# Kernel tuning notes

Hardware: AMD Instinct MI355X
Metric: run time of the kernel (lower is better)

## Reference

```python
import jax, jax.numpy as jnp
import numpy as np

K, M, N = 8, 1024, 1024  # bits, in_features, out_features (nf)
B_, S_ = 4, 2048

def setup_inputs() -> dict:
    key = jax.random.key(0)
    k1, k2, k3, k4 = jax.random.split(key, 4)
    x = jax.random.normal(k1, (B_, S_, M), dtype=jnp.float32)
    # per-bit +/-1 sign matrices, stored as float (module casts int8 -> x.dtype)
    binary = jnp.where(jax.random.normal(k2, (K, M, N)) > 0, 1.0, -1.0).astype(jnp.float32)
    # positive per-bit, per-output-channel scales (sup decomposition yields positives)
    scale = jax.random.uniform(k3, (K, 1, N), dtype=jnp.float32, minval=0.01, maxval=1.0)
    bias = jax.random.normal(k4, (N,), dtype=jnp.float32)
    return {"x": x, "binary": binary, "scale": scale, "bias": bias}

def reference(x, binary, scale, bias):
    size_out = x.shape[:-1] + (N,)
    x2 = x.reshape(-1, x.shape[-1])                 # [T, m]
    # k separate dense matmuls against +/-1 matrices: [k, T, n]
    xk = jnp.einsum('tm,kmn->ktn', x2, binary)
    out = jnp.sum(xk * scale, axis=0)               # per-bit scale then sum over bits
    out = out + bias
    return out.reshape(size_out)
```

## Files before the change

### kernel.cpp

```cpp
#include <hip/hip_runtime.h>
#include <cstdint>

#define TDIM 8192
#define MDIM 1024
#define NDIM 1024
#define KBITS 8
#define BK 64
#define TT 64
#define TN 128

typedef __bf16 bf16x8 __attribute__((ext_vector_type(8)));
typedef float f32x4 __attribute__((ext_vector_type(4)));
typedef float f32x16 __attribute__((ext_vector_type(16)));

#define GAS(p) ((__attribute__((address_space(1))) void*)(uintptr_t)(p))
#define LAS(p) ((__attribute__((address_space(3))) void*)(uintptr_t)(p))

__device__ __forceinline__ unsigned short f2bf(float f) {
    union { float f; unsigned u; } v; v.f = f;
    unsigned r = v.u + 0x7fffu + ((v.u >> 16) & 1u);
    return (unsigned short)(r >> 16);
}

__global__ __launch_bounds__(256) void prep_kernel(const float* __restrict__ x,
                                                   unsigned short* __restrict__ xb,
                                                   const float* __restrict__ binary,
                                                   const float* __restrict__ scale,
                                                   unsigned short* __restrict__ wtr) {
    __shared__ float tile[32][33];
    const int tid = threadIdx.x;
    if (blockIdx.x >= 1024) {
        size_t idx = ((size_t)(blockIdx.x - 1024) * 256 + tid) * 8;
        float4 a = *(const float4*)(x + idx);
        float4 b = *(const float4*)(x + idx + 4);
        uint4 o;
        o.x = (unsigned)f2bf(a.x) | ((unsigned)f2bf(a.y) << 16);
        o.y = (unsigned)f2bf(a.z) | ((unsigned)f2bf(a.w) << 16);
        o.z = (unsigned)f2bf(b.x) | ((unsigned)f2bf(b.y) << 16);
        o.w = (unsigned)f2bf(b.z) | ((unsigned)f2bf(b.w) << 16);
        *(uint4*)(xb + idx) = o;
        return;
    }
    const int n0 = (blockIdx.x & 31) * 32;
    const int m0 = (blockIdx.x >> 5) * 32;
    const int r = tid >> 3;
    const int cn = (tid & 7) * 4;
    f32x4 acc = {0.f, 0.f, 0.f, 0.f};
#pragma unroll
    for (int k = 0; k < KBITS; ++k) {
        f32x4 v = *(const f32x4*)(binary + ((size_t)k * MDIM + m0 + r) * NDIM + n0 + cn);
        f32x4 s = *(const f32x4*)(scale + (size_t)k * NDIM + n0 + cn);
        acc += v * s;
    }
#pragma unroll
    for (int e = 0; e < 4; ++e) tile[cn + e][r] = acc[e];
    __syncthreads();
    const int rn = tid >> 3;
    const int cm = (tid & 7) * 4;
    ushort4 o4;
    o4.x = f2bf(tile[rn][cm + 0]);
    o4.y = f2bf(tile[rn][cm + 1]);
    o4.z = f2bf(tile[rn][cm + 2]);
    o4.w = f2bf(tile[rn][cm + 3]);
    *(ushort4*)(wtr + (size_t)(n0 + rn) * MDIM + m0 + cm) = o4;
}

__global__ __launch_bounds__(256, 4) void gemm_kernel(const unsigned short* __restrict__ xb,
                                                      const unsigned short* __restrict__ wtr,
                                                      const float* __restrict__ bias,
                                                      float* __restrict__ out) {
    __shared__ __attribute__((aligned(16))) unsigned short sA[TT * BK];
    __shared__ __attribute__((aligned(16))) unsigned short sB[TN * BK];

    const int tid = threadIdx.x;
    const int lane = tid & 63;
    const int wv = tid >> 6;
    const int wrow = wv >> 1;
    const int wcol = wv & 1;
    const int lr = lane & 31;
    const int half = lane >> 5;

    const int t0 = blockIdx.x * TT;
    const int n0 = blockIdx.y * TN;

    const unsigned short* srcA[2];
    unsigned short* dstA[2];
#pragma unroll
    for (int j = 0; j < 2; ++j) {
        int s = tid + j * 256;
        int r = s >> 3;
        int g = (s & 7) ^ (r & 7);
        srcA[j] = xb + (size_t)(t0 + r) * MDIM + g * 8;
        dstA[j] = sA + s * 8;
    }
    const unsigned short* srcB[4];
    unsigned short* dstB[4];
#pragma unroll
    for (int j = 0; j < 4; ++j) {
        int s = tid + j * 256;
        int r = s >> 3;
        int g = (s & 7) ^ (r & 7);
        srcB[j] = wtr + (size_t)(n0 + r) * MDIM + g * 8;
        dstB[j] = sB + s * 8;
    }

    int a_off[4], b_off[4][2];
#pragma unroll
    for (int c = 0; c < 4; ++c) {
        int m = wrow * 32 + lr;
        a_off[c] = (m * 8 + ((c * 2 + half) ^ (m & 7))) * 8;
#pragma unroll
        for (int j = 0; j < 2; ++j) {
            int n = wcol * 64 + j * 32 + lr;
            b_off[c][j] = (n * 8 + ((c * 2 + half) ^ (n & 7))) * 8;
        }
    }

    f32x16 acc[2];
#pragma unroll
    for (int j = 0; j < 2; ++j)
#pragma unroll
        for (int r = 0; r < 16; ++r) acc[j][r] = 0.f;

    for (int k0 = 0; k0 < MDIM; k0 += BK) {
#pragma unroll
        for (int j = 0; j < 2; ++j)
            __builtin_amdgcn_global_load_lds(GAS(srcA[j] + k0), LAS(dstA[j]), 16, 0, 0);
#pragma unroll
        for (int j = 0; j < 4; ++j)
            __builtin_amdgcn_global_load_lds(GAS(srcB[j] + k0), LAS(dstB[j]), 16, 0, 0);
        __syncthreads();

#pragma unroll
        for (int c = 0; c < 4; ++c) {
            bf16x8 af = *(const bf16x8*)(sA + a_off[c]);
            bf16x8 b0 = *(const bf16x8*)(sB + b_off[c][0]);
            bf16x8 b1 = *(const bf16x8*)(sB + b_off[c][1]);
            acc[0] = __builtin_amdgcn_mfma_f32_32x32x16_bf16(af, b0, acc[0], 0, 0, 0);
            acc[1] = __builtin_amdgcn_mfma_f32_32x32x16_bf16(af, b1, acc[1], 0, 0, 0);
        }
        __syncthreads();
    }

#pragma unroll
    for (int j = 0; j < 2; ++j) {
        const int n = n0 + wcol * 64 + j * 32 + lr;
        const float bv = bias[n];
#pragma unroll
        for (int r = 0; r < 16; ++r) {
            const int t = t0 + wrow * 32 + (r & 3) + 8 * (r >> 2) + 4 * half;
            out[(size_t)t * NDIM + n] = acc[j][r] + bv;
        }
    }
}

extern "C" void kernel_launch(void* const* d_in, const int* in_sizes, int n_in,
                              void* d_out, int out_size, void* d_ws, size_t ws_size,
                              hipStream_t stream) {
    const float* x      = (const float*)d_in[0];
    const float* binary = (const float*)d_in[1];
    const float* scale  = (const float*)d_in[2];
    const float* bias   = (const float*)d_in[3];
    float* out = (float*)d_out;

    unsigned short* xb  = (unsigned short*)d_ws;
    unsigned short* wtr = xb + (size_t)TDIM * MDIM;

    prep_kernel<<<1024 + 4096, 256, 0, stream>>>(x, xb, binary, scale, wtr);
    gemm_kernel<<<dim3(TDIM / TT, NDIM / TN), 256, 0, stream>>>(xb, wtr, bias, out);
}
```

Baseline: 128.0 us.

## Fuse x fp32-to-bf16 conversion into GEMM A-tile loading

```diff
diff --git a/kernel.cpp b/kernel.cpp
--- a/kernel.cpp
+++ b/kernel.cpp
@@ -22,25 +22,11 @@
     return (unsigned short)(r >> 16);
 }
 
-__global__ __launch_bounds__(256) void prep_kernel(const float* __restrict__ x,
-                                                   unsigned short* __restrict__ xb,
-                                                   const float* __restrict__ binary,
-                                                   const float* __restrict__ scale,
-                                                   unsigned short* __restrict__ wtr) {
+__global__ __launch_bounds__(256) void wfold_kernel(const float* __restrict__ binary,
+                                                    const float* __restrict__ scale,
+                                                    unsigned short* __restrict__ wtr) {
     __shared__ float tile[32][33];
     const int tid = threadIdx.x;
-    if (blockIdx.x >= 1024) {
-        size_t idx = ((size_t)(blockIdx.x - 1024) * 256 + tid) * 8;
-        float4 a = *(const float4*)(x + idx);
-        float4 b = *(const float4*)(x + idx + 4);
-        uint4 o;
-        o.x = (unsigned)f2bf(a.x) | ((unsigned)f2bf(a.y) << 16);
-        o.y = (unsigned)f2bf(a.z) | ((unsigned)f2bf(a.w) << 16);
-        o.z = (unsigned)f2bf(b.x) | ((unsigned)f2bf(b.y) << 16);
-        o.w = (unsigned)f2bf(b.z) | ((unsigned)f2bf(b.w) << 16);
-        *(uint4*)(xb + idx) = o;
-        return;
-    }
     const int n0 = (blockIdx.x & 31) * 32;
     const int m0 = (blockIdx.x >> 5) * 32;
     const int r = tid >> 3;
@@ -65,11 +51,11 @@
     *(ushort4*)(wtr + (size_t)(n0 + rn) * MDIM + m0 + cm) = o4;
 }
 
-__global__ __launch_bounds__(256, 4) void gemm_kernel(const unsigned short* __restrict__ xb,
+__global__ __launch_bounds__(256, 4) void gemm_kernel(const float* __restrict__ x,
                                                       const unsigned short* __restrict__ wtr,
                                                       const float* __restrict__ bias,
                                                       float* __restrict__ out) {
-    __shared__ __attribute__((aligned(16))) unsigned short sA[TT * BK];
+    __shared__ __attribute__((aligned(16))) float sAf[TT * BK];
     __shared__ __attribute__((aligned(16))) unsigned short sB[TN * BK];
 
     const int tid = threadIdx.x;
@@ -83,15 +69,15 @@
     const int t0 = blockIdx.x * TT;
     const int n0 = blockIdx.y * TN;
 
-    const unsigned short* srcA[2];
-    unsigned short* dstA[2];
+    const float* srcA[4];
+    float* dstA[4];
 #pragma unroll
-    for (int j = 0; j < 2; ++j) {
+    for (int j = 0; j < 4; ++j) {
         int s = tid + j * 256;
-        int r = s >> 3;
-        int g = (s & 7) ^ (r & 7);
-        srcA[j] = xb + (size_t)(t0 + r) * MDIM + g * 8;
-        dstA[j] = sA + s * 8;
+        int r = s >> 4;
+        int g = (s & 15) ^ (r & 15);
+        srcA[j] = x + (size_t)(t0 + r) * MDIM + g * 4;
+        dstA[j] = sAf + s * 4;
     }
     const unsigned short* srcB[4];
     unsigned short* dstB[4];
@@ -104,11 +90,12 @@
         dstB[j] = sB + s * 8;
     }
 
-    int a_off[4], b_off[4][2];
+    const int mrow = wrow * 32 + lr;
+    int a0_off[4], a1_off[4], b_off[4][2];
 #pragma unroll
     for (int c = 0; c < 4; ++c) {
-        int m = wrow * 32 + lr;
-        a_off[c] = (m * 8 + ((c * 2 + half) ^ (m & 7))) * 8;
+        a0_off[c] = mrow * 64 + ((4 * c + 2 * half) ^ (mrow & 15)) * 4;
+        a1_off[c] = mrow * 64 + ((4 * c + 2 * half + 1) ^ (mrow & 15)) * 4;
 #pragma unroll
         for (int j = 0; j < 2; ++j) {
             int n = wcol * 64 + j * 32 + lr;
@@ -124,7 +111,7 @@
 
     for (int k0 = 0; k0 < MDIM; k0 += BK) {
 #pragma unroll
-        for (int j = 0; j < 2; ++j)
+        for (int j = 0; j < 4; ++j)
             __builtin_amdgcn_global_load_lds(GAS(srcA[j] + k0), LAS(dstA[j]), 16, 0, 0);
 #pragma unroll
         for (int j = 0; j < 4; ++j)
@@ -133,11 +120,23 @@
 
 #pragma unroll
         for (int c = 0; c < 4; ++c) {
-            bf16x8 af = *(const bf16x8*)(sA + a_off[c]);
+            f32x4 va = *(const f32x4*)(sAf + a0_off[c]);
+            f32x4 vb = *(const f32x4*)(sAf + a1_off[c]);
+            union { unsigned u[4]; bf16x8 v; } af;
+            union { float f; unsigned u; } e0, e1;
+            e0.f = va[0]; e1.f = va[1];
+            af.u[0] = __builtin_amdgcn_perm(e1.u, e0.u, 0x07060302);
+            e0.f = va[2]; e1.f = va[3];
+            af.u[1] = __builtin_amdgcn_perm(e1.u, e0.u, 0x07060302);
+            e0.f = vb[0]; e1.f = vb[1];
+            af.u[2] = __builtin_amdgcn_perm(e1.u, e0.u, 0x07060302);
+            e0.f = vb[2]; e1.f = vb[3];
+            af.u[3] = __builtin_amdgcn_perm(e1.u, e0.u, 0x07060302);
+
             bf16x8 b0 = *(const bf16x8*)(sB + b_off[c][0]);
             bf16x8 b1 = *(const bf16x8*)(sB + b_off[c][1]);
-            acc[0] = __builtin_amdgcn_mfma_f32_32x32x16_bf16(af, b0, acc[0], 0, 0, 0);
-            acc[1] = __builtin_amdgcn_mfma_f32_32x32x16_bf16(af, b1, acc[1], 0, 0, 0);
+            acc[0] = __builtin_amdgcn_mfma_f32_32x32x16_bf16(af.v, b0, acc[0], 0, 0, 0);
+            acc[1] = __builtin_amdgcn_mfma_f32_32x32x16_bf16(af.v, b1, acc[1], 0, 0, 0);
         }
         __syncthreads();
     }
@@ -163,9 +162,8 @@
     const float* bias   = (const float*)d_in[3];
     float* out = (float*)d_out;
 
-    unsigned short* xb  = (unsigned short*)d_ws;
-    unsigned short* wtr = xb + (size_t)TDIM * MDIM;
+    unsigned short* wtr = (unsigned short*)d_ws;
 
-    prep_kernel<<<1024 + 4096, 256, 0, stream>>>(x, xb, binary, scale, wtr);
-    gemm_kernel<<<dim3(TDIM / TT, NDIM / TN), 256, 0, stream>>>(xb, wtr, bias, out);
+    wfold_kernel<<<1024, 256, 0, stream>>>(binary, scale, wtr);
+    gemm_kernel<<<dim3(TDIM / TT, NDIM / TN), 256, 0, stream>>>(x, wtr, bias, out);
 }
```

Result: no change. 129.1 us (+0.9%).

## Pre-swizzle activations into MFMA fragment layout and double-buffer weight tiles

Applied to the files above, without the earlier changes.

```diff
diff --git a/kernel.cpp b/kernel.cpp
--- a/kernel.cpp
+++ b/kernel.cpp
@@ -6,7 +6,7 @@
 #define NDIM 1024
 #define KBITS 8
 #define BK 64
-#define TT 64
+#define TT 128
 #define TN 128
 
 typedef __bf16 bf16x8 __attribute__((ext_vector_type(8)));
@@ -30,15 +30,25 @@
     __shared__ float tile[32][33];
     const int tid = threadIdx.x;
     if (blockIdx.x >= 1024) {
-        size_t idx = ((size_t)(blockIdx.x - 1024) * 256 + tid) * 8;
-        float4 a = *(const float4*)(x + idx);
-        float4 b = *(const float4*)(x + idx + 4);
-        uint4 o;
-        o.x = (unsigned)f2bf(a.x) | ((unsigned)f2bf(a.y) << 16);
-        o.y = (unsigned)f2bf(a.z) | ((unsigned)f2bf(a.w) << 16);
-        o.z = (unsigned)f2bf(b.x) | ((unsigned)f2bf(b.y) << 16);
-        o.w = (unsigned)f2bf(b.z) | ((unsigned)f2bf(b.w) << 16);
-        *(uint4*)(xb + idx) = o;
+        const int b = blockIdx.x - 1024;
+        const int tb = b >> 3;
+        const int gchunk = b & 7;
+#pragma unroll
+        for (int p = 0; p < 2; ++p) {
+            const int flat = tid + p * 256;
+            const int goff = (flat & 7) | (p << 3);
+            const int r = (flat >> 3) & 31;
+            const int g = gchunk * 16 + goff;
+            const float* src = x + ((size_t)tb * 32 + r) * MDIM + g * 8;
+            float4 a = *(const float4*)(src);
+            float4 c = *(const float4*)(src + 4);
+            uint4 o;
+            o.x = (unsigned)f2bf(a.x) | ((unsigned)f2bf(a.y) << 16);
+            o.y = (unsigned)f2bf(a.z) | ((unsigned)f2bf(a.w) << 16);
+            o.z = (unsigned)f2bf(c.x) | ((unsigned)f2bf(c.y) << 16);
+            o.w = (unsigned)f2bf(c.z) | ((unsigned)f2bf(c.w) << 16);
+            *(uint4*)(xb + (((size_t)tb * 128 + g) * 32 + r) * 8) = o;
+        }
         return;
     }
     const int n0 = (blockIdx.x & 31) * 32;
@@ -65,12 +75,11 @@
     *(ushort4*)(wtr + (size_t)(n0 + rn) * MDIM + m0 + cm) = o4;
 }
 
-__global__ __launch_bounds__(256, 4) void gemm_kernel(const unsigned short* __restrict__ xb,
-                                                      const unsigned short* __restrict__ wtr,
-                                                      const float* __restrict__ bias,
-                                                      float* __restrict__ out) {
-    __shared__ __attribute__((aligned(16))) unsigned short sA[TT * BK];
-    __shared__ __attribute__((aligned(16))) unsigned short sB[TN * BK];
+__global__ __launch_bounds__(256) void gemm_kernel(const unsigned short* __restrict__ xb,
+                                                   const unsigned short* __restrict__ wtr,
+                                                   const float* __restrict__ bias,
+                                                   float* __restrict__ out) {
+    __shared__ __attribute__((aligned(16))) unsigned short sB[2 * TN * BK];
 
     const int tid = threadIdx.x;
     const int lane = tid & 63;
@@ -83,16 +92,6 @@
     const int t0 = blockIdx.x * TT;
     const int n0 = blockIdx.y * TN;
 
-    const unsigned short* srcA[2];
-    unsigned short* dstA[2];
-#pragma unroll
-    for (int j = 0; j < 2; ++j) {
-        int s = tid + j * 256;
-        int r = s >> 3;
-        int g = (s & 7) ^ (r & 7);
-        srcA[j] = xb + (size_t)(t0 + r) * MDIM + g * 8;
-        dstA[j] = sA + s * 8;
-    }
     const unsigned short* srcB[4];
     unsigned short* dstB[4];
 #pragma unroll
@@ -104,40 +103,55 @@
         dstB[j] = sB + s * 8;
     }
 
-    int a_off[4], b_off[4][2];
+    const unsigned short* aptr[2];
 #pragma unroll
-    for (int c = 0; c < 4; ++c) {
-        int m = wrow * 32 + lr;
-        a_off[c] = (m * 8 + ((c * 2 + half) ^ (m & 7))) * 8;
+    for (int i = 0; i < 2; ++i) {
+        size_t tb = (size_t)(t0 >> 5) + wrow * 2 + i;
+        aptr[i] = xb + (tb * 128 + half) * 256 + lr * 8;
+    }
+
+    int b_off[4][2];
+#pragma unroll
+    for (int c = 0; c < 4; ++c)
 #pragma unroll
         for (int j = 0; j < 2; ++j) {
             int n = wcol * 64 + j * 32 + lr;
-            b_off[c][j] = (n * 8 + ((c * 2 + half) ^ (n & 7))) * 8;
+            b_off[c][j] = (n * 8 + ((2 * c + half) ^ (n & 7))) * 8;
         }
-    }
 
-    f32x16 acc[2];
+    f32x16 acc[2][2];
 #pragma unroll
-    for (int j = 0; j < 2; ++j)
-#pragma unroll
-        for (int r = 0; r < 16; ++r) acc[j][r] = 0.f;
-
-    for (int k0 = 0; k0 < MDIM; k0 += BK) {
+    for (int i = 0; i < 2; ++i)
 #pragma unroll
         for (int j = 0; j < 2; ++j)
-            __builtin_amdgcn_global_load_lds(GAS(srcA[j] + k0), LAS(dstA[j]), 16, 0, 0);
 #pragma unroll
-        for (int j = 0; j < 4; ++j)
-            __builtin_amdgcn_global_load_lds(GAS(srcB[j] + k0), LAS(dstB[j]), 16, 0, 0);
-        __syncthreads();
+            for (int r = 0; r < 16; ++r) acc[i][j][r] = 0.f;
 
 #pragma unroll
+    for (int j = 0; j < 4; ++j)
+        __builtin_amdgcn_global_load_lds(GAS(srcB[j]), LAS(dstB[j]), 16, 0, 0);
+    __syncthreads();
+
+    for (int it = 0; it < MDIM / BK; ++it) {
+        const int buf = (it & 1) << 13;
+        if (it < MDIM / BK - 1) {
+            const int nbuf = 8192 - buf;
+            const int kof = (it + 1) * BK;
+#pragma unroll
+            for (int j = 0; j < 4; ++j)
+                __builtin_amdgcn_global_load_lds(GAS(srcB[j] + kof), LAS(dstB[j] + nbuf), 16, 0, 0);
+        }
+        const int aof = it * (BK * 32);
+#pragma unroll
         for (int c = 0; c < 4; ++c) {
-            bf16x8 af = *(const bf16x8*)(sA + a_off[c]);
-            bf16x8 b0 = *(const bf16x8*)(sB + b_off[c][0]);
-            bf16x8 b1 = *(const bf16x8*)(sB + b_off[c][1]);
-            acc[0] = __builtin_amdgcn_mfma_f32_32x32x16_bf16(af, b0, acc[0], 0, 0, 0);
-            acc[1] = __builtin_amdgcn_mfma_f32_32x32x16_bf16(af, b1, acc[1], 0, 0, 0);
+            bf16x8 a0 = *(const bf16x8*)(aptr[0] + aof + c * 512);
+            bf16x8 a1 = *(const bf16x8*)(aptr[1] + aof + c * 512);
+            bf16x8 b0 = *(const bf16x8*)(sB + buf + b_off[c][0]);
+            bf16x8 b1 = *(const bf16x8*)(sB + buf + b_off[c][1]);
+            acc[0][0] = __builtin_amdgcn_mfma_f32_32x32x16_bf16(a0, b0, acc[0][0], 0, 0, 0);
+            acc[1][0] = __builtin_amdgcn_mfma_f32_32x32x16_bf16(a1, b0, acc[1][0], 0, 0, 0);
+            acc[0][1] = __builtin_amdgcn_mfma_f32_32x32x16_bf16(a0, b1, acc[0][1], 0, 0, 0);
+            acc[1][1] = __builtin_amdgcn_mfma_f32_32x32x16_bf16(a1, b1, acc[1][1], 0, 0, 0);
         }
         __syncthreads();
     }
@@ -147,9 +161,13 @@
         const int n = n0 + wcol * 64 + j * 32 + lr;
         const float bv = bias[n];
 #pragma unroll
-        for (int r = 0; r < 16; ++r) {
-            const int t = t0 + wrow * 32 + (r & 3) + 8 * (r >> 2) + 4 * half;
-            out[(size_t)t * NDIM + n] = acc[j][r] + bv;
+        for (int i = 0; i < 2; ++i) {
+            const int tb = t0 + wrow * 64 + i * 32;
+#pragma unroll
+            for (int r = 0; r < 16; ++r) {
+                const int t = tb + (r & 3) + 8 * (r >> 2) + 4 * half;
+                out[(size_t)t * NDIM + n] = acc[i][j][r] + bv;
+            }
         }
     }
 }
@@ -166,6 +184,6 @@
     unsigned short* xb  = (unsigned short*)d_ws;
     unsigned short* wtr = xb + (size_t)TDIM * MDIM;
 
-    prep_kernel<<<1024 + 4096, 256, 0, stream>>>(x, xb, binary, scale, wtr);
+    prep_kernel<<<1024 + 2048, 256, 0, stream>>>(x, xb, binary, scale, wtr);
     gemm_kernel<<<dim3(TDIM / TT, NDIM / TN), 256, 0, stream>>>(xb, wtr, bias, out);
 }
```

Result: no change. 127.2 us (-0.6%).
